# Kernel optimization log

Measured on AMD Instinct MI355X. Metric: run time of the kernel, lower is better.

Reference implementation:

```python
import jax, jax.numpy as jnp
import numpy as np

B, T, D = 64, 512, 1024  # batch, step_dim, feature_dim


def setup_inputs() -> dict:
    key = jax.random.key(0)
    k1, k2, k3, k4, k5 = jax.random.split(key, 5)
    x = jax.random.normal(k1, (B, T, D), dtype=jnp.float32)
    mask = jax.random.randint(k2, (B, T), 0, 2).astype(bool)
    mask = mask.at[:, 0].set(True)  # guarantee >=1 valid token per row
    # xavier_uniform bounds
    w_bound = float(np.sqrt(6.0 / (D + D)))
    c_bound = float(np.sqrt(6.0 / (T + 1)))
    weight = jax.random.uniform(k3, (D, D), minval=-w_bound, maxval=w_bound, dtype=jnp.float32)
    context_vector = jax.random.uniform(k4, (T, 1), minval=-c_bound, maxval=c_bound, dtype=jnp.float32)
    b = jnp.zeros((T,), dtype=jnp.float32)
    return {"x": x, "mask": mask, "weight": weight, "context_vector": context_vector, "b": b}


def reference(x, mask, weight, context_vector, b):
    # batched bilinear scores: eij[b,t,s] = x[b,t,:] @ W @ x[b,s,:]^T
    xw = jnp.einsum('btd,de->bte', x, weight)          # [B,T,D]
    eij = jnp.einsum('bte,bse->bts', xw, x)            # [B,T,T]
    # bias over last axis (matches view(-1, T) + b), tanh
    eij = jnp.tanh(eij + b)                            # [B,T,T]
    # context-vector reduction over last axis -> [B,T]
    scores = jnp.einsum('bts,s->bt', eij, context_vector[:, 0])
    # masked softmax over T
    scores = jnp.where(mask, scores, -jnp.inf)
    a = jax.nn.softmax(scores, axis=1)                 # [B,T]
    # weighted sum of inputs -> [B,D]
    out = jnp.einsum('btd,bt->bd', x, a)
    return (out, a)
```

## Files before the change

### kernel.cpp

```cpp
#include <hip/hip_runtime.h>
#include <hip/hip_bf16.h>
#include <math.h>

#define B_ 64
#define T_ 512
#define D_ 1024
#define M_ (B_*T_)

typedef unsigned short u16;
typedef __attribute__((ext_vector_type(8))) _Float16 f16x8;
typedef __attribute__((ext_vector_type(4))) float f32x4;

__device__ __forceinline__ u16 f2h(float f) {
  union { _Float16 h; u16 u; } v;
  v.h = (_Float16)f;
  return v.u;
}

__device__ __forceinline__ float h2f(u16 u) {
  union { u16 u; _Float16 h; } v;
  v.u = u;
  return (float)v.h;
}

__device__ __forceinline__ float fast_tanh(float x) {
  return 1.0f - 2.0f / (__expf(2.0f * x) + 1.0f);
}

__device__ __forceinline__ void gll16(const void* g, void* l) {
  __builtin_amdgcn_global_load_lds(
      (const __attribute__((address_space(1))) unsigned int*)g,
      (__attribute__((address_space(3))) unsigned int*)l, 16, 0, 0);
}

__global__ __launch_bounds__(256) void cvt_kernel(const float4* __restrict__ x,
                                                  ushort4* __restrict__ xh,
                                                  const float* __restrict__ W,
                                                  u16* __restrict__ wt) {
  __shared__ float tile[32][33];
  const int bid = blockIdx.x;
  if (bid < 32768) {
    int i = bid * 256 + threadIdx.x;
    float4 v = x[i];
    ushort4 o;
    o.x = f2h(v.x); o.y = f2h(v.y); o.z = f2h(v.z); o.w = f2h(v.w);
    xh[i] = o;
  } else {
    const int tb = bid - 32768;
    const int n0 = (tb & 31) * 32, k0 = (tb >> 5) * 32;
    const int tx = threadIdx.x & 31, ty = threadIdx.x >> 5;
#pragma unroll
    for (int ph = 0; ph < 4; ph++)
      tile[ty + ph * 8][tx] = W[(k0 + ty + ph * 8) * D_ + n0 + tx];
    __syncthreads();
#pragma unroll
    for (int ph = 0; ph < 4; ph++)
      wt[(long)(n0 + ty + ph * 8) * D_ + k0 + tx] = f2h(tile[tx][ty + ph * 8]);
  }
}

__global__ __launch_bounds__(256, 2) void gemm1_kernel(const u16* __restrict__ xh,
                                                       const u16* __restrict__ wt,
                                                       u16* __restrict__ xw) {
  __shared__ u16 As[256 * 64];
  __shared__ u16 Bs[128 * 64];
  f32x4 acc[8][4] = {};
  const int tid = threadIdx.x;
  const int bx = blockIdx.x;
  const int xcd = bx & 7, j = bx >> 3;
  const int mt = xcd * 16 + (j >> 3);
  const int nt = j & 7;
  const long m0 = (long)mt * 256;
  const long n0 = (long)nt * 128;
  const u16* Abase = xh + m0 * D_;
  const u16* Bbase = wt + n0 * D_;

  const int wave = tid >> 6, lane = tid & 63;
  const int p = lane & 7, rl = lane >> 3;

  const u16* gA[8]; u16* lA[8];
#pragma unroll
  for (int i = 0; i < 8; i++) {
    int g = wave * 8 + i;
    int r = g * 8 + rl;
    int c = (p - (r >> 1)) & 7;
    gA[i] = Abase + (long)r * D_ + c * 8;
    lA[i] = As + g * 512;
  }
  const u16* gB[4]; u16* lB[4];
#pragma unroll
  for (int i = 0; i < 4; i++) {
    int g = wave * 4 + i;
    int r = g * 8 + rl;
    int c = (p - (r >> 1)) & 7;
    gB[i] = Bbase + (long)r * D_ + c * 8;
    lB[i] = Bs + g * 512;
  }

  const int wrow = (wave >> 1) * 128, wcol = (wave & 1) * 64;
  const int lm = lane & 15, qd = lane >> 4;
  const u16* ra = As + (wrow + lm) * 64;
  const u16* rb = Bs + (wcol + lm) * 64;
  const int pk0 = ((qd + (lm >> 1)) & 7) * 8;
  const int pk1 = ((qd + 4 + (lm >> 1)) & 7) * 8;

  for (int kt = 0; kt < D_; kt += 64) {
#pragma unroll
    for (int i = 0; i < 8; i++) { gll16(gA[i], lA[i]); gA[i] += 64; }
#pragma unroll
    for (int i = 0; i < 4; i++) { gll16(gB[i], lB[i]); gB[i] += 64; }
    __syncthreads();
#pragma unroll
    for (int kk = 0; kk < 2; kk++) {
      const int pk = kk ? pk1 : pk0;
      f16x8 af[8], bfr[4];
#pragma unroll
      for (int i = 0; i < 8; i++) af[i] = *(const f16x8*)(ra + i * 16 * 64 + pk);
#pragma unroll
      for (int i = 0; i < 4; i++) bfr[i] = *(const f16x8*)(rb + i * 16 * 64 + pk);
#pragma unroll
      for (int mi = 0; mi < 8; mi++)
#pragma unroll
        for (int ni = 0; ni < 4; ni++)
          acc[mi][ni] = __builtin_amdgcn_mfma_f32_16x16x32_f16(af[mi], bfr[ni], acc[mi][ni], 0, 0, 0);
    }
    __syncthreads();
  }

  const int lm2 = lane & 15, qd2 = lane >> 4;
#pragma unroll
  for (int mi = 0; mi < 8; mi++)
#pragma unroll
    for (int ni = 0; ni < 4; ni++) {
      long m = m0 + wrow + mi * 16 + qd2 * 4;
      long n = n0 + wcol + ni * 16 + lm2;
      u16* ptr = xw + m * D_ + n;
#pragma unroll
      for (int r = 0; r < 4; r++) ptr[(long)r * D_] = f2h(acc[mi][ni][r]);
    }
}

__device__ __forceinline__ void gemm_core128(const u16* __restrict__ Abase,
                                             const u16* __restrict__ Bbase, int K,
                                             u16* As, u16* Bs, int tid, f32x4 acc[4][4]) {
  const int wave = tid >> 6, lane = tid & 63;
  const int swz_c = ((lane & 3) - ((lane >> 3) & 3)) & 3;
  const int rin = lane >> 2;
  const u16* gA[2]; u16* lA[2];
  const u16* gB[2]; u16* lB[2];
#pragma unroll
  for (int j = 0; j < 2; j++) {
    int ci = wave * 2 + j;
    gA[j] = Abase + (long)(ci * 16 + rin) * K + swz_c * 8;
    lA[j] = As + ci * 512;
    gB[j] = Bbase + (long)(ci * 16 + rin) * K + swz_c * 8;
    lB[j] = Bs + ci * 512;
  }
  const int wrow = (wave >> 1) * 64, wcol = (wave & 1) * 64;
  const int lm = lane & 15, qd = lane >> 4;
  const int swz_r = ((qd + (lm >> 1)) & 3) * 8;
  const u16* ra = As + (wrow + lm) * 32 + swz_r;
  const u16* rb = Bs + (wcol + lm) * 32 + swz_r;

  for (int kt = 0; kt < K; kt += 32) {
#pragma unroll
    for (int j = 0; j < 2; j++) {
      gll16(gA[j], lA[j]); gA[j] += 32;
      gll16(gB[j], lB[j]); gB[j] += 32;
    }
    __syncthreads();
    f16x8 af[4], bfr[4];
#pragma unroll
    for (int i = 0; i < 4; i++) {
      af[i] = *(const f16x8*)(ra + i * 512);
      bfr[i] = *(const f16x8*)(rb + i * 512);
    }
#pragma unroll
    for (int mi = 0; mi < 4; mi++)
#pragma unroll
      for (int ni = 0; ni < 4; ni++)
        acc[mi][ni] = __builtin_amdgcn_mfma_f32_16x16x32_f16(af[mi], bfr[ni], acc[mi][ni], 0, 0, 0);
    __syncthreads();
  }
}

__global__ __launch_bounds__(256, 4) void gemm2_kernel(const u16* __restrict__ xw,
                                                       const u16* __restrict__ xh,
                                                       const float* __restrict__ bias,
                                                       const float* __restrict__ cv,
                                                       float* __restrict__ scores_part) {
  __shared__ u16 As[128 * 32], Bs[128 * 32];
  f32x4 acc[4][4] = {};
  const int bx = blockIdx.x;
  const int xcd = bx & 7, j = bx >> 3;
  const int bb = xcd * 8 + (j >> 4);
  const int tile = j & 15;
  const int tt = tile >> 2, st = tile & 3;
  const int tid = threadIdx.x;
  const long arow = (long)bb * T_ + tt * 128;
  const long brow = (long)bb * T_ + st * 128;
  gemm_core128(xw + arow * D_, xh + brow * D_, D_, As, Bs, tid, acc);

  const int wave = tid >> 6, lane = tid & 63;
  const int wrow = (wave >> 1) * 64, wcol = (wave & 1) * 64;
  const int lm = lane & 15, qd = lane >> 4;
  float cvv[4], bv[4];
#pragma unroll
  for (int ni = 0; ni < 4; ni++) {
    int s = st * 128 + wcol + ni * 16 + lm;
    cvv[ni] = cv[s];
    bv[ni] = bias[s];
  }
  const int plane = st * 2 + (wave & 1);
  float* dst = scores_part + plane * (B_ * T_) + bb * T_ + tt * 128;
#pragma unroll
  for (int mi = 0; mi < 4; mi++) {
#pragma unroll
    for (int r = 0; r < 4; r++) {
      float p = 0.f;
#pragma unroll
      for (int ni = 0; ni < 4; ni++) p += fast_tanh(acc[mi][ni][r] + bv[ni]) * cvv[ni];
      p += __shfl_xor(p, 1); p += __shfl_xor(p, 2);
      p += __shfl_xor(p, 4); p += __shfl_xor(p, 8);
      if (lm == 0) dst[wrow + mi * 16 + qd * 4 + r] = p;
    }
  }
}

__global__ __launch_bounds__(256) void sm_wsum_kernel(const float* __restrict__ sp,
                                                      const unsigned char* __restrict__ m8,
                                                      const u16* __restrict__ xh,
                                                      float* __restrict__ a_out,
                                                      float* __restrict__ out) {
  __shared__ float a_sh[512];
  __shared__ float red[8];
  __shared__ int nonz;
  __shared__ float4 lred[4][64];
  const int b = blockIdx.x, dq = blockIdx.y, tid = threadIdx.x;
  const int w = tid >> 6, ln = tid & 63;
  if (tid == 0) nonz = 0;
  __syncthreads();
  {
    unsigned char c = m8[tid * 4 + 1] | m8[tid * 4 + 2] | m8[tid * 4 + 3] |
                      m8[(tid + 256) * 4 + 1] | m8[(tid + 256) * 4 + 2] | m8[(tid + 256) * 4 + 3];
    if (c) atomicOr(&nonz, 1);
  }
  __syncthreads();
  const bool is_i32 = (nonz == 0);
  float v[2]; bool valid[2];
#pragma unroll
  for (int h = 0; h < 2; h++) {
    int t = tid + h * 256;
    int idx = b * T_ + t;
    valid[h] = is_i32 ? (m8[(long)idx * 4] != 0) : (m8[idx] != 0);
    float s = 0.f;
#pragma unroll
    for (int pl = 0; pl < 8; pl++) s += sp[pl * (B_ * T_) + idx];
    v[h] = valid[h] ? s : -INFINITY;
  }
  float m = fmaxf(v[0], v[1]);
#pragma unroll
  for (int o = 32; o > 0; o >>= 1) m = fmaxf(m, __shfl_xor(m, o));
  if (ln == 0) red[w] = m;
  __syncthreads();
  const float rowmax = fmaxf(fmaxf(red[0], red[1]), fmaxf(red[2], red[3]));
  float e0 = valid[0] ? expf(v[0] - rowmax) : 0.f;
  float e1 = valid[1] ? expf(v[1] - rowmax) : 0.f;
  float ss = e0 + e1;
#pragma unroll
  for (int o = 32; o > 0; o >>= 1) ss += __shfl_xor(ss, o);
  if (ln == 0) red[4 + w] = ss;
  __syncthreads();
  const float tot = red[4] + red[5] + red[6] + red[7];
  const float a0 = e0 / tot, a1 = e1 / tot;
  a_sh[tid] = a0; a_sh[tid + 256] = a1;
  if (dq == 0) {
    a_out[b * T_ + tid] = a0;
    a_out[b * T_ + tid + 256] = a1;
  }
  __syncthreads();
  const int d0 = dq * 256 + ln * 4;
  const u16* xp = xh + (long)b * T_ * D_ + d0;
  float4 acc = make_float4(0.f, 0.f, 0.f, 0.f);
  for (int i = 0; i < 128; i++) {
    int t = w * 128 + i;
    float av = a_sh[t];
    ushort4 xv = *(const ushort4*)(xp + (long)t * D_);
    acc.x += av * h2f(xv.x); acc.y += av * h2f(xv.y);
    acc.z += av * h2f(xv.z); acc.w += av * h2f(xv.w);
  }
  lred[w][ln] = acc;
  __syncthreads();
  if (w == 0) {
    float4 s0 = lred[0][ln], s1 = lred[1][ln], s2 = lred[2][ln], s3 = lred[3][ln];
    float4 s;
    s.x = s0.x + s1.x + s2.x + s3.x;
    s.y = s0.y + s1.y + s2.y + s3.y;
    s.z = s0.z + s1.z + s2.z + s3.z;
    s.w = s0.w + s1.w + s2.w + s3.w;
    *(float4*)(out + (long)b * D_ + d0) = s;
  }
}

extern "C" void kernel_launch(void* const* d_in, const int* in_sizes, int n_in,
                              void* d_out, int out_size, void* d_ws, size_t ws_size,
                              hipStream_t stream) {
  const float* x = (const float*)d_in[0];
  const unsigned char* mask = (const unsigned char*)d_in[1];
  const float* W = (const float*)d_in[2];
  const float* cv = (const float*)d_in[3];
  const float* bias = (const float*)d_in[4];

  float* out = (float*)d_out;
  float* a_out = out + (size_t)B_ * D_;

  char* ws = (char*)d_ws;
  u16* xh = (u16*)(ws);
  u16* wt = (u16*)(ws + 67108864);
  float* scores_part = (float*)(ws + 67108864);
  u16* xw = (u16*)(ws + 69206016);

  cvt_kernel<<<32768 + 1024, 256, 0, stream>>>((const float4*)x, (ushort4*)xh, W, wt);
  gemm1_kernel<<<1024, 256, 0, stream>>>(xh, wt, xw);
  gemm2_kernel<<<1024, 256, 0, stream>>>(xw, xh, bias, cv, scores_part);
  sm_wsum_kernel<<<dim3(B_, 4), 256, 0, stream>>>(scores_part, mask, xh, a_out, out);
}
```

Baseline: 323.4 us.

## Unify GEMMs on BK=64 core with improved LDS swizzle

Factors the BK=64 GEMM main loop into a templated core shared by both GEMMs. The second GEMM moves from a BK=32 loop to BK=64, which halves its barrier count per K and doubles its LDS footprint. The swizzle is changed to also mix in the row parity, to cut LDS bank conflicts on fragment reads. gemm1's launch bound rises to 3 waves' worth of blocks per CU and gemm2 drops its occupancy hint, which may change register allocation.

Result: slower. 385.2 us (+19.1%).

```diff
diff --git a/kernel.cpp b/kernel.cpp
--- a/kernel.cpp
+++ b/kernel.cpp
@@ -59,7 +59,64 @@
   }
 }
 
-__global__ __launch_bounds__(256, 2) void gemm1_kernel(const u16* __restrict__ xh,
+template <int MI>
+__device__ __forceinline__ void gemm_core_bk64(const u16* __restrict__ Abase,
+                                               const u16* __restrict__ Bbase,
+                                               u16* As, u16* Bs, int tid,
+                                               f32x4 (&acc)[MI][4]) {
+  const int wave = tid >> 6, lane = tid & 63;
+  const int p = lane & 7, rl = lane >> 3;
+  const u16* gA[MI]; u16* lA[MI];
+#pragma unroll
+  for (int i = 0; i < MI; i++) {
+    int g = wave * MI + i;
+    int r = g * 8 + rl;
+    int c = (p - ((r >> 1) + 4 * (r & 1))) & 7;
+    gA[i] = Abase + (long)r * D_ + c * 8;
+    lA[i] = As + g * 512;
+  }
+  const u16* gB[4]; u16* lB[4];
+#pragma unroll
+  for (int i = 0; i < 4; i++) {
+    int g = wave * 4 + i;
+    int r = g * 8 + rl;
+    int c = (p - ((r >> 1) + 4 * (r & 1))) & 7;
+    gB[i] = Bbase + (long)r * D_ + c * 8;
+    lB[i] = Bs + g * 512;
+  }
+  const int wrow = (wave >> 1) * (MI * 16), wcol = (wave & 1) * 64;
+  const int lm = lane & 15, qd = lane >> 4;
+  const int h = (lm >> 1) + 4 * (lm & 1);
+  const int pk0 = ((qd + h) & 7) * 8;
+  const int pk1 = ((qd + 4 + h) & 7) * 8;
+  const u16* ra = As + (wrow + lm) * 64;
+  const u16* rb = Bs + (wcol + lm) * 64;
+
+  for (int kt = 0; kt < D_; kt += 64) {
+#pragma unroll
+    for (int i = 0; i < MI; i++) { gll16(gA[i], lA[i]); gA[i] += 64; }
+#pragma unroll
+    for (int i = 0; i < 4; i++) { gll16(gB[i], lB[i]); gB[i] += 64; }
+    __syncthreads();
+#pragma unroll
+    for (int kk = 0; kk < 2; kk++) {
+      const int pk = kk ? pk1 : pk0;
+      f16x8 af[MI], bfr[4];
+#pragma unroll
+      for (int i = 0; i < MI; i++) af[i] = *(const f16x8*)(ra + i * 1024 + pk);
+#pragma unroll
+      for (int i = 0; i < 4; i++) bfr[i] = *(const f16x8*)(rb + i * 1024 + pk);
+#pragma unroll
+      for (int mi = 0; mi < MI; mi++)
+#pragma unroll
+        for (int ni = 0; ni < 4; ni++)
+          acc[mi][ni] = __builtin_amdgcn_mfma_f32_16x16x32_f16(af[mi], bfr[ni], acc[mi][ni], 0, 0, 0);
+    }
+    __syncthreads();
+  }
+}
+
+__global__ __launch_bounds__(256, 3) void gemm1_kernel(const u16* __restrict__ xh,
                                                        const u16* __restrict__ wt,
                                                        u16* __restrict__ xw) {
   __shared__ u16 As[256 * 64];
@@ -72,124 +129,30 @@
   const int nt = j & 7;
   const long m0 = (long)mt * 256;
   const long n0 = (long)nt * 128;
-  const u16* Abase = xh + m0 * D_;
-  const u16* Bbase = wt + n0 * D_;
+  gemm_core_bk64<8>(xh + m0 * D_, wt + n0 * D_, As, Bs, tid, acc);
 
   const int wave = tid >> 6, lane = tid & 63;
-  const int p = lane & 7, rl = lane >> 3;
-
-  const u16* gA[8]; u16* lA[8];
-#pragma unroll
-  for (int i = 0; i < 8; i++) {
-    int g = wave * 8 + i;
-    int r = g * 8 + rl;
-    int c = (p - (r >> 1)) & 7;
-    gA[i] = Abase + (long)r * D_ + c * 8;
-    lA[i] = As + g * 512;
-  }
-  const u16* gB[4]; u16* lB[4];
-#pragma unroll
-  for (int i = 0; i < 4; i++) {
-    int g = wave * 4 + i;
-    int r = g * 8 + rl;
-    int c = (p - (r >> 1)) & 7;
-    gB[i] = Bbase + (long)r * D_ + c * 8;
-    lB[i] = Bs + g * 512;
-  }
-
   const int wrow = (wave >> 1) * 128, wcol = (wave & 1) * 64;
   const int lm = lane & 15, qd = lane >> 4;
-  const u16* ra = As + (wrow + lm) * 64;
-  const u16* rb = Bs + (wcol + lm) * 64;
-  const int pk0 = ((qd + (lm >> 1)) & 7) * 8;
-  const int pk1 = ((qd + 4 + (lm >> 1)) & 7) * 8;
-
-  for (int kt = 0; kt < D_; kt += 64) {
-#pragma unroll
-    for (int i = 0; i < 8; i++) { gll16(gA[i], lA[i]); gA[i] += 64; }
-#pragma unroll
-    for (int i = 0; i < 4; i++) { gll16(gB[i], lB[i]); gB[i] += 64; }
-    __syncthreads();
-#pragma unroll
-    for (int kk = 0; kk < 2; kk++) {
-      const int pk = kk ? pk1 : pk0;
-      f16x8 af[8], bfr[4];
-#pragma unroll
-      for (int i = 0; i < 8; i++) af[i] = *(const f16x8*)(ra + i * 16 * 64 + pk);
-#pragma unroll
-      for (int i = 0; i < 4; i++) bfr[i] = *(const f16x8*)(rb + i * 16 * 64 + pk);
-#pragma unroll
-      for (int mi = 0; mi < 8; mi++)
-#pragma unroll
-        for (int ni = 0; ni < 4; ni++)
-          acc[mi][ni] = __builtin_amdgcn_mfma_f32_16x16x32_f16(af[mi], bfr[ni], acc[mi][ni], 0, 0, 0);
-    }
-    __syncthreads();
-  }
-
-  const int lm2 = lane & 15, qd2 = lane >> 4;
 #pragma unroll
   for (int mi = 0; mi < 8; mi++)
 #pragma unroll
     for (int ni = 0; ni < 4; ni++) {
-      long m = m0 + wrow + mi * 16 + qd2 * 4;
-      long n = n0 + wcol + ni * 16 + lm2;
+      long m = m0 + wrow + mi * 16 + qd * 4;
+      long n = n0 + wcol + ni * 16 + lm;
       u16* ptr = xw + m * D_ + n;
 #pragma unroll
       for (int r = 0; r < 4; r++) ptr[(long)r * D_] = f2h(acc[mi][ni][r]);
     }
 }
 
-__device__ __forceinline__ void gemm_core128(const u16* __restrict__ Abase,
-                                             const u16* __restrict__ Bbase, int K,
-                                             u16* As, u16* Bs, int tid, f32x4 acc[4][4]) {
-  const int wave = tid >> 6, lane = tid & 63;
-  const int swz_c = ((lane & 3) - ((lane >> 3) & 3)) & 3;
-  const int rin = lane >> 2;
-  const u16* gA[2]; u16* lA[2];
-  const u16* gB[2]; u16* lB[2];
-#pragma unroll
-  for (int j = 0; j < 2; j++) {
-    int ci = wave * 2 + j;
-    gA[j] = Abase + (long)(ci * 16 + rin) * K + swz_c * 8;
-    lA[j] = As + ci * 512;
-    gB[j] = Bbase + (long)(ci * 16 + rin) * K + swz_c * 8;
-    lB[j] = Bs + ci * 512;
-  }
-  const int wrow = (wave >> 1) * 64, wcol = (wave & 1) * 64;
-  const int lm = lane & 15, qd = lane >> 4;
-  const int swz_r = ((qd + (lm >> 1)) & 3) * 8;
-  const u16* ra = As + (wrow + lm) * 32 + swz_r;
-  const u16* rb = Bs + (wcol + lm) * 32 + swz_r;
-
-  for (int kt = 0; kt < K; kt += 32) {
-#pragma unroll
-    for (int j = 0; j < 2; j++) {
-      gll16(gA[j], lA[j]); gA[j] += 32;
-      gll16(gB[j], lB[j]); gB[j] += 32;
-    }
-    __syncthreads();
-    f16x8 af[4], bfr[4];
-#pragma unroll
-    for (int i = 0; i < 4; i++) {
-      af[i] = *(const f16x8*)(ra + i * 512);
-      bfr[i] = *(const f16x8*)(rb + i * 512);
-    }
-#pragma unroll
-    for (int mi = 0; mi < 4; mi++)
-#pragma unroll
-      for (int ni = 0; ni < 4; ni++)
-        acc[mi][ni] = __builtin_amdgcn_mfma_f32_16x16x32_f16(af[mi], bfr[ni], acc[mi][ni], 0, 0, 0);
-    __syncthreads();
-  }
-}
-
-__global__ __launch_bounds__(256, 4) void gemm2_kernel(const u16* __restrict__ xw,
-                                                       const u16* __restrict__ xh,
-                                                       const float* __restrict__ bias,
-                                                       const float* __restrict__ cv,
-                                                       float* __restrict__ scores_part) {
-  __shared__ u16 As[128 * 32], Bs[128 * 32];
+__global__ __launch_bounds__(256) void gemm2_kernel(const u16* __restrict__ xw,
+                                                    const u16* __restrict__ xh,
+                                                    const float* __restrict__ bias,
+                                                    const float* __restrict__ cv,
+                                                    float* __restrict__ scores_part) {
+  __shared__ u16 As[128 * 64];
+  __shared__ u16 Bs[128 * 64];
   f32x4 acc[4][4] = {};
   const int bx = blockIdx.x;
   const int xcd = bx & 7, j = bx >> 3;
@@ -199,7 +162,7 @@
   const int tid = threadIdx.x;
   const long arow = (long)bb * T_ + tt * 128;
   const long brow = (long)bb * T_ + st * 128;
-  gemm_core128(xw + arow * D_, xh + brow * D_, D_, As, Bs, tid, acc);
+  gemm_core_bk64<4>(xw + arow * D_, xh + brow * D_, As, Bs, tid, acc);
 
   const int wave = tid >> 6, lane = tid & 63;
   const int wrow = (wave >> 1) * 64, wcol = (wave & 1) * 64;
```
